# Kernel optimization log

Hardware: AMD Instinct MI355X
Metric: run time of the kernel (lower is better)

## Reference

```python
import jax, jax.numpy as jnp
import numpy as np

HEADS = 8
D_MODEL = 512
HEAD_DIM = D_MODEL // HEADS


def setup_inputs() -> dict:
    key = jax.random.key(0)
    ks = jax.random.split(key, 13)
    B, S, D = 8, 1024, D_MODEL
    scale = 1.0 / np.sqrt(D)
    x = jax.random.normal(ks[0], (B, S, D), dtype=jnp.float32)
    names = ['cq', 'ck', 'cv', 'pq', 'pk', 'pv']
    inp = {'x': x}
    for i, n in enumerate(names):
        inp['W_' + n] = jax.random.normal(ks[1 + 2 * i], (D, D), dtype=jnp.float32) * scale
        inp['b_' + n] = jax.random.normal(ks[2 + 2 * i], (D,), dtype=jnp.float32) * 0.01
    return inp


def reference(x, W_cq, b_cq, W_ck, b_ck, W_cv, b_cv, W_pq, b_pq, W_pk, b_pk, W_pv, b_pv):
    # x: [N, S, D]. Fused common + personal QKV: (x@Wc + bc) + (x@Wp + bp)
    N, S, D = x.shape
    q = x @ (W_cq + W_pq) + (b_cq + b_pq)  # [N, S, D]
    k = x @ (W_ck + W_pk) + (b_ck + b_pk)
    v = x @ (W_cv + W_pv) + (b_cv + b_pv)
    q = q.reshape(N, S, HEADS, HEAD_DIM)
    k = k.reshape(N, S, HEADS, HEAD_DIM)
    v = v.reshape(N, S, HEADS, HEAD_DIM)
    # NOTE: original scales by sqrt(d_model), not sqrt(head_dim)
    energy = jnp.einsum('nqhd,nkhd->nhqk', q, k) / jnp.sqrt(jnp.asarray(D, x.dtype))
    attn = jax.nn.softmax(energy, axis=-1)  # [N, H, Q, K]
    out = jnp.einsum('nhqk,nkhd->nqhd', attn, v).reshape(N, S, D)
    return out
```

## Files before the change

### kernel.cpp

```cpp
#include <hip/hip_runtime.h>

#define B_   8
#define S_   1024
#define D_   512
#define H_   8
#define HD_  64
#define NT_  (B_ * S_)
#define QSCALE_ 0.06376387f
#define C4_    5.7707802f

typedef _Float16 f16;
typedef _Float16 f16x4 __attribute__((ext_vector_type(4)));
typedef _Float16 f16x8 __attribute__((ext_vector_type(8)));
typedef float    f32x4 __attribute__((ext_vector_type(4)));

#define GLOAD_LDS16(g, l) \
    __builtin_amdgcn_global_load_lds( \
        (const __attribute__((address_space(1))) unsigned int*)(g), \
        (__attribute__((address_space(3))) unsigned int*)(l), 16, 0, 0)

#define MFMA16(a, b, c) __builtin_amdgcn_mfma_f32_16x16x32_f16(a, b, c, 0, 0, 0)


__global__ __launch_bounds__(256) void prep_fused(
    const float* __restrict__ x, f16* __restrict__ xh_t,
    const float* __restrict__ Wcq, const float* __restrict__ Wck, const float* __restrict__ Wcv,
    const float* __restrict__ Wpq, const float* __restrict__ Wpk, const float* __restrict__ Wpv,
    f16* __restrict__ Bt_t)
{
    __shared__ float tile[64][68];
    const int tid = threadIdx.x;

    if (blockIdx.x < 1024) {
        const int mtile = blockIdx.x >> 4;
        const int ktile = blockIdx.x & 15;
        f16* dst = xh_t + ((size_t)mtile * 16 + ktile) * 4096;
#pragma unroll
        for (int half = 0; half < 2; ++half) {
            const int q = half * 256 + tid;
            const int r = q >> 2;
            const int c = q & 3;
            const float* src = x + (size_t)(mtile * 128 + r) * D_ + ktile * 32 + c * 8;
            float4 a = *(const float4*)(src);
            float4 b = *(const float4*)(src + 4);
            f16x8 o = { (f16)a.x, (f16)a.y, (f16)a.z, (f16)a.w,
                        (f16)b.x, (f16)b.y, (f16)b.z, (f16)b.w };
            *(f16x8*)(dst + c * 1024 + r * 8) = o;
        }
        return;
    }

    const int wk = blockIdx.x - 1024;
    const int k0 = (wk & 7) * 64;
    const int n0 = (wk >> 3) * 64;
    const int g  = n0 >> 9;
    const int c0 = n0 & 511;
    const float* Wc = (g == 0) ? Wcq : (g == 1) ? Wck : Wcv;
    const float* Wp = (g == 0) ? Wpq : (g == 1) ? Wpk : Wpv;

#pragma unroll
    for (int it = 0; it < 4; ++it) {
        int row = it * 16 + (tid >> 4);
        int c4  = (tid & 15) * 4;
        float4 a = *(const float4*)(Wc + (size_t)(k0 + row) * D_ + c0 + c4);
        float4 b = *(const float4*)(Wp + (size_t)(k0 + row) * D_ + c0 + c4);
        tile[row][c4 + 0] = a.x + b.x;
        tile[row][c4 + 1] = a.y + b.y;
        tile[row][c4 + 2] = a.z + b.z;
        tile[row][c4 + 3] = a.w + b.w;
    }
    __syncthreads();

    const int ntile = n0 >> 7;
    const int rbase = n0 & 64;
#pragma unroll
    for (int it = 0; it < 2; ++it) {
        int nr = it * 32 + (tid >> 3);
        int kc = (tid & 7) * 8;
        f16x8 o;
#pragma unroll
        for (int j = 0; j < 8; ++j) o[j] = (f16)tile[kc + j][nr];
        const int kt = (k0 + kc) >> 5;
        const int c  = (kc >> 3) & 3;
        const int r  = rbase + nr;
        *(f16x8*)(Bt_t + ((size_t)ntile * 16 + kt) * 4096 + c * 1024 + r * 8) = o;
    }
}

__global__ __launch_bounds__(256) void qkv_gemm(
    const f16* __restrict__ xh_t, const f16* __restrict__ Bt_t,
    const float* __restrict__ bcq, const float* __restrict__ bck, const float* __restrict__ bcv,
    const float* __restrict__ bpq, const float* __restrict__ bpk, const float* __restrict__ bpv,
    f16* __restrict__ Qh, f16* __restrict__ Kws, f16* __restrict__ Vws)
{
    __shared__ __align__(16) char smem_raw[36864];

    const int bid   = blockIdx.x;
    const int xcd   = bid & 7;
    const int idx   = bid >> 3;
    const int mtile = xcd * 8 + (idx & 7);
    const int ntile = idx >> 3;
    const int m0 = mtile * 128;
    const int n0 = ntile * 128;

    const int tid  = threadIdx.x;
    const int lane = tid & 63;
    const int wave = tid >> 6;
    const int wr = wave >> 1, wc = wave & 1;
    const int lo4 = lane & 15, hi4 = lane >> 4;

    const f16* gA = xh_t + (size_t)mtile * 16 * 4096;
    const f16* gB = Bt_t + (size_t)ntile * 16 * 4096;

#define STAGE(bufsel, kt) do { \
        f16* _A = (f16*)(smem_raw + (bufsel) * 16384); \
        f16* _B = (f16*)(smem_raw + (bufsel) * 16384 + 8192); \
        GLOAD_LDS16(gA + (kt) * 4096 + tid * 8,         _A + tid * 8);         \
        GLOAD_LDS16(gA + (kt) * 4096 + (tid + 256) * 8, _A + (tid + 256) * 8); \
        GLOAD_LDS16(gB + (kt) * 4096 + tid * 8,         _B + tid * 8);         \
        GLOAD_LDS16(gB + (kt) * 4096 + (tid + 256) * 8, _B + (tid + 256) * 8); \
    } while (0)

    f32x4 acc[4][4];
#pragma unroll
    for (int i = 0; i < 4; ++i)
#pragma unroll
        for (int j = 0; j < 4; ++j) acc[i][j] = (f32x4){0.f, 0.f, 0.f, 0.f};

    STAGE(0, 0);
    asm volatile("s_waitcnt vmcnt(0)" ::: "memory");
    __syncthreads();

    for (int t = 0; t < 16; ++t) {
        const int cur = t & 1;
        if (t < 15) STAGE(cur ^ 1, t + 1);

        const f16* Ab = (const f16*)(smem_raw + cur * 16384);
        const f16* Bb = (const f16*)(smem_raw + cur * 16384 + 8192);
        f16x8 a[4], b[4];
#pragma unroll
        for (int i = 0; i < 4; ++i)
            a[i] = *(const f16x8*)(Ab + hi4 * 1024 + (wr * 64 + i * 16 + lo4) * 8);
#pragma unroll
        for (int j = 0; j < 4; ++j)
            b[j] = *(const f16x8*)(Bb + hi4 * 1024 + (wc * 64 + j * 16 + lo4) * 8);
#pragma unroll
        for (int i = 0; i < 4; ++i)
#pragma unroll
            for (int j = 0; j < 4; ++j)
                acc[i][j] = MFMA16(a[i], b[j], acc[i][j]);

        asm volatile("s_waitcnt vmcnt(0)" ::: "memory");
        __syncthreads();
    }
#undef STAGE

    const int g = n0 >> 9;
    const float* bc = (g == 0) ? bcq : (g == 1) ? bck : bcv;
    const float* bp = (g == 0) ? bpq : (g == 1) ? bpk : bpv;

    const int colb = n0 + wc * 64;
    const int h    = (colb & 511) >> 6;
    const int rowb = m0 + wr * 64;
    const int bb   = rowb >> 10;
    const int s0   = rowb & 1023;

    float bias[4];
#pragma unroll
    for (int j = 0; j < 4; ++j) {
        const int cg = (colb + j * 16 + lo4) & 511;
        bias[j] = bc[cg] + bp[cg];
    }

    f16* Cs = (f16*)smem_raw + wave * 4608;
    const size_t bhbase = (size_t)(bb * H_ + h) * 65536;

    if (g == 2) {
#pragma unroll
        for (int i = 0; i < 4; ++i)
#pragma unroll
            for (int j = 0; j < 4; ++j) {
                f16x4 v = { (f16)(acc[i][j][0] + bias[j]), (f16)(acc[i][j][1] + bias[j]),
                            (f16)(acc[i][j][2] + bias[j]), (f16)(acc[i][j][3] + bias[j]) };
                *(f16x4*)(Cs + (j * 16 + lo4) * 72 + i * 16 + hi4 * 4) = v;
            }
        asm volatile("s_waitcnt lgkmcnt(0)" ::: "memory");
        __builtin_amdgcn_sched_barrier(0);
        const size_t tbase = bhbase + (size_t)(s0 >> 6) * 4096;
#pragma unroll
        for (int it = 0; it < 8; ++it) {
            const int d  = it * 8 + (lane >> 3);
            const int cs = lane & 7;
            f16x8 chunk = *(const f16x8*)(Cs + d * 72 + cs * 8);
            *(f16x8*)(Vws + tbase + d * 64 + ((cs ^ (d & 7)) << 3)) = chunk;
        }
    } else {
        const float scale = (g == 0) ? QSCALE_ : 1.f;
#pragma unroll
        for (int i = 0; i < 4; ++i)
#pragma unroll
            for (int j = 0; j < 4; ++j)
#pragma unroll
                for (int r = 0; r < 4; ++r)
                    Cs[(i * 16 + hi4 * 4 + r) * 72 + j * 16 + lo4] =
                        (f16)((acc[i][j][r] + bias[j]) * scale);
        asm volatile("s_waitcnt lgkmcnt(0)" ::: "memory");
        __builtin_amdgcn_sched_barrier(0);
#pragma unroll
        for (int it = 0; it < 8; ++it) {
            const int rr = it * 8 + (lane >> 3);
            const int ci = lane & 7;
            f16x8 chunk = *(const f16x8*)(Cs + rr * 72 + ci * 8);
            if (g == 0) {
                *(f16x8*)(Qh + bhbase + (size_t)(s0 + rr) * 64 + ci * 8) = chunk;
            } else {
                const size_t tbase = bhbase + (size_t)(s0 >> 6) * 4096;
                *(f16x8*)(Kws + tbase + rr * 64 + ((ci ^ (rr & 7)) << 3)) = chunk;
            }
        }
    }
}

__global__ __launch_bounds__(256) void attn_fwd(
    const f16* __restrict__ Qh, const f16* __restrict__ Kws,
    const f16* __restrict__ Vws, float* __restrict__ out)
{
    __shared__ __align__(16) f16 Ks[2][4096];
    __shared__ __align__(16) f16 Vs[2][4096];
    __shared__ __align__(16) f16 Ps[4][32 * 72];

    const int b0 = blockIdx.x;
    const int bh = (b0 & 7) * 8 + ((b0 >> 3) & 7);
    const int qt = b0 >> 6;

    const int wave = threadIdx.x >> 6;
    const int lane = threadIdx.x & 63;
    const int lo4 = lane & 15, hi4 = lane >> 4;
    const int q0 = qt * 128 + wave * 32;

    const f16* Qp = Qh  + (size_t)bh * 65536;
    const f16* Kp = Kws + (size_t)bh * 65536;
    const f16* Vp = Vws + (size_t)bh * 65536;
    f16* Pw = &Ps[wave][0];

    f16x8 aq[2][2];
#pragma unroll
    for (int qg = 0; qg < 2; ++qg)
#pragma unroll
        for (int hh = 0; hh < 2; ++hh)
            aq[qg][hh] = *(const f16x8*)(Qp + (q0 + qg * 16 + lo4) * 64 + hh * 32 + hi4 * 8);

    f32x4 o[2][4];
    float l[2][4];
#pragma unroll
    for (int qg = 0; qg < 2; ++qg)
#pragma unroll
        for (int dt = 0; dt < 4; ++dt) {
            o[qg][dt] = (f32x4){0.f, 0.f, 0.f, 0.f};
            l[qg][dt] = 0.f;
        }

    const int soff = threadIdx.x * 8;
    GLOAD_LDS16(Kp + soff,        &Ks[0][soff]);
    GLOAD_LDS16(Kp + 2048 + soff, &Ks[0][2048 + soff]);
    GLOAD_LDS16(Vp + soff,        &Vs[0][soff]);
    GLOAD_LDS16(Vp + 2048 + soff, &Vs[0][2048 + soff]);
    asm volatile("s_waitcnt vmcnt(0)" ::: "memory");
    __syncthreads();

    for (int t = 0; t < 16; ++t) {
        const int cur = t & 1;
        if (t < 15) {
            const f16* Kn = Kp + (t + 1) * 4096;
            const f16* Vn = Vp + (t + 1) * 4096;
            GLOAD_LDS16(Kn + soff,        &Ks[cur ^ 1][soff]);
            GLOAD_LDS16(Kn + 2048 + soff, &Ks[cur ^ 1][2048 + soff]);
            GLOAD_LDS16(Vn + soff,        &Vs[cur ^ 1][soff]);
            GLOAD_LDS16(Vn + 2048 + soff, &Vs[cur ^ 1][2048 + soff]);
        }
        const f16* Kc = &Ks[cur][0];
        const f16* Vc = &Vs[cur][0];

#pragma unroll
        for (int f = 0; f < 4; ++f) {
            const int c = f * 16 + lo4;
            f16x8 bk0 = *(const f16x8*)(Kc + c * 64 + ((hi4 ^ (c & 7)) << 3));
            f16x8 bk1 = *(const f16x8*)(Kc + c * 64 + (((4 + hi4) ^ (c & 7)) << 3));
#pragma unroll
            for (int qg = 0; qg < 2; ++qg) {
                f32x4 sc = (f32x4){0.f, 0.f, 0.f, 0.f};
                sc = MFMA16(aq[qg][0], bk0, sc);
                sc = MFMA16(aq[qg][1], bk1, sc);
#pragma unroll
                for (int r = 0; r < 4; ++r) {
                    float p = __builtin_amdgcn_exp2f(sc[r] - C4_);
                    l[qg][r] += p;
                    Pw[(qg * 16 + hi4 * 4 + r) * 72 + f * 16 + lo4] = (f16)p;
                }
            }
        }
        asm volatile("s_waitcnt lgkmcnt(0)" ::: "memory");
        __builtin_amdgcn_sched_barrier(0);

        f16x8 ap[2][2];
#pragma unroll
        for (int qg = 0; qg < 2; ++qg) {
            ap[qg][0] = *(const f16x8*)(Pw + (qg * 16 + lo4) * 72 + hi4 * 8);
            ap[qg][1] = *(const f16x8*)(Pw + (qg * 16 + lo4) * 72 + 32 + hi4 * 8);
        }
#pragma unroll
        for (int dt = 0; dt < 4; ++dt) {
            const int d = dt * 16 + lo4;
            f16x8 bv0 = *(const f16x8*)(Vc + d * 64 + ((hi4 ^ (d & 7)) << 3));
            f16x8 bv1 = *(const f16x8*)(Vc + d * 64 + (((4 + hi4) ^ (d & 7)) << 3));
#pragma unroll
            for (int qg = 0; qg < 2; ++qg) {
                o[qg][dt] = MFMA16(ap[qg][0], bv0, o[qg][dt]);
                o[qg][dt] = MFMA16(ap[qg][1], bv1, o[qg][dt]);
            }
        }

        asm volatile("s_waitcnt vmcnt(0)" ::: "memory");
        __syncthreads();
    }

    const int b = bh >> 3;
    const int h = bh & 7;
#pragma unroll
    for (int qg = 0; qg < 2; ++qg)
#pragma unroll
        for (int r = 0; r < 4; ++r) {
            float lv = l[qg][r];
            lv += __shfl_xor(lv, 1);
            lv += __shfl_xor(lv, 2);
            lv += __shfl_xor(lv, 4);
            lv += __shfl_xor(lv, 8);
            const float inv = 1.f / lv;
            const int s_idx = q0 + qg * 16 + hi4 * 4 + r;
            float* op = out + ((size_t)(b * S_ + s_idx)) * D_ + h * HD_;
#pragma unroll
            for (int dt = 0; dt < 4; ++dt)
                op[dt * 16 + lo4] = o[qg][dt][r] * inv;
        }
}

extern "C" void kernel_launch(void* const* d_in, const int* in_sizes, int n_in,
                              void* d_out, int out_size, void* d_ws, size_t ws_size,
                              hipStream_t stream)
{
    const float* x   = (const float*)d_in[0];
    const float* Wcq = (const float*)d_in[1];
    const float* bcq = (const float*)d_in[2];
    const float* Wck = (const float*)d_in[3];
    const float* bck = (const float*)d_in[4];
    const float* Wcv = (const float*)d_in[5];
    const float* bcv = (const float*)d_in[6];
    const float* Wpq = (const float*)d_in[7];
    const float* bpq = (const float*)d_in[8];
    const float* Wpk = (const float*)d_in[9];
    const float* bpk = (const float*)d_in[10];
    const float* Wpv = (const float*)d_in[11];
    const float* bpv = (const float*)d_in[12];

    f16* ws = (f16*)d_ws;
    f16* xh_t = ws;
    f16* Bt_t = xh_t + (size_t)64 * 16 * 4096;
    f16* Qh   = Bt_t + (size_t)12 * 16 * 4096;
    f16* Kws  = Qh + (size_t)64 * 65536;
    f16* Vws  = Kws + (size_t)64 * 65536;
    float* o = (float*)d_out;

    prep_fused<<<1216, 256, 0, stream>>>(x, xh_t, Wcq, Wck, Wcv, Wpq, Wpk, Wpv, Bt_t);
    qkv_gemm<<<768, 256, 0, stream>>>(xh_t, Bt_t, bcq, bck, bcv, bpq, bpk, bpv,
                                      Qh, Kws, Vws);
    attn_fwd<<<512, 256, 0, stream>>>(Qh, Kws, Vws, o);
}
```

Baseline: 58.02 us.

## Store V transposed and load PV operands directly from global into registers

The QKV GEMM now writes V as a plain per-head transposed [d][s] array instead of swizzled 64x64 tiles. The attention kernel drops the LDS double buffer for V and has each wave read its V operand fragments straight from global memory at the start of each key tile. This frees LDS and cuts the async copy traffic, but every wave now issues its own uncached-in-LDS global loads for V. Those loads are exposed in the loop unless the QK phase hides their latency, and they are redundant across the four waves.

```diff
diff --git a/kernel.cpp b/kernel.cpp
--- a/kernel.cpp
+++ b/kernel.cpp
@@ -91,7 +91,7 @@
     const f16* __restrict__ xh_t, const f16* __restrict__ Bt_t,
     const float* __restrict__ bcq, const float* __restrict__ bck, const float* __restrict__ bcv,
     const float* __restrict__ bpq, const float* __restrict__ bpk, const float* __restrict__ bpv,
-    f16* __restrict__ Qh, f16* __restrict__ Kws, f16* __restrict__ Vws)
+    f16* __restrict__ Qh, f16* __restrict__ Kws, f16* __restrict__ Vt)
 {
     __shared__ __align__(16) char smem_raw[36864];
 
@@ -186,13 +186,12 @@
             }
         asm volatile("s_waitcnt lgkmcnt(0)" ::: "memory");
         __builtin_amdgcn_sched_barrier(0);
-        const size_t tbase = bhbase + (size_t)(s0 >> 6) * 4096;
 #pragma unroll
         for (int it = 0; it < 8; ++it) {
             const int d  = it * 8 + (lane >> 3);
             const int cs = lane & 7;
             f16x8 chunk = *(const f16x8*)(Cs + d * 72 + cs * 8);
-            *(f16x8*)(Vws + tbase + d * 64 + ((cs ^ (d & 7)) << 3)) = chunk;
+            *(f16x8*)(Vt + bhbase + (size_t)d * 1024 + s0 + cs * 8) = chunk;
         }
     } else {
         const float scale = (g == 0) ? QSCALE_ : 1.f;
@@ -223,10 +222,9 @@
 
 __global__ __launch_bounds__(256) void attn_fwd(
     const f16* __restrict__ Qh, const f16* __restrict__ Kws,
-    const f16* __restrict__ Vws, float* __restrict__ out)
+    const f16* __restrict__ Vt, float* __restrict__ out)
 {
     __shared__ __align__(16) f16 Ks[2][4096];
-    __shared__ __align__(16) f16 Vs[2][4096];
     __shared__ __align__(16) f16 Ps[4][32 * 72];
 
     const int b0 = blockIdx.x;
@@ -240,7 +238,7 @@
 
     const f16* Qp = Qh  + (size_t)bh * 65536;
     const f16* Kp = Kws + (size_t)bh * 65536;
-    const f16* Vp = Vws + (size_t)bh * 65536;
+    const f16* Vp = Vt  + (size_t)bh * 65536;
     f16* Pw = &Ps[wave][0];
 
     f16x8 aq[2][2];
@@ -263,8 +261,6 @@
     const int soff = threadIdx.x * 8;
     GLOAD_LDS16(Kp + soff,        &Ks[0][soff]);
     GLOAD_LDS16(Kp + 2048 + soff, &Ks[0][2048 + soff]);
-    GLOAD_LDS16(Vp + soff,        &Vs[0][soff]);
-    GLOAD_LDS16(Vp + 2048 + soff, &Vs[0][2048 + soff]);
     asm volatile("s_waitcnt vmcnt(0)" ::: "memory");
     __syncthreads();
 
@@ -272,14 +268,18 @@
         const int cur = t & 1;
         if (t < 15) {
             const f16* Kn = Kp + (t + 1) * 4096;
-            const f16* Vn = Vp + (t + 1) * 4096;
             GLOAD_LDS16(Kn + soff,        &Ks[cur ^ 1][soff]);
             GLOAD_LDS16(Kn + 2048 + soff, &Ks[cur ^ 1][2048 + soff]);
-            GLOAD_LDS16(Vn + soff,        &Vs[cur ^ 1][soff]);
-            GLOAD_LDS16(Vn + 2048 + soff, &Vs[cur ^ 1][2048 + soff]);
-        }
+        }
+        f16x8 bv[4][2];
+#pragma unroll
+        for (int dt = 0; dt < 4; ++dt)
+#pragma unroll
+            for (int hh = 0; hh < 2; ++hh)
+                bv[dt][hh] = *(const f16x8*)(Vp + (size_t)(dt * 16 + lo4) * 1024
+                                             + t * 64 + hh * 32 + hi4 * 8);
+
         const f16* Kc = &Ks[cur][0];
-        const f16* Vc = &Vs[cur][0];
 
 #pragma unroll
         for (int f = 0; f < 4; ++f) {
@@ -309,16 +309,12 @@
             ap[qg][1] = *(const f16x8*)(Pw + (qg * 16 + lo4) * 72 + 32 + hi4 * 8);
         }
 #pragma unroll
-        for (int dt = 0; dt < 4; ++dt) {
-            const int d = dt * 16 + lo4;
-            f16x8 bv0 = *(const f16x8*)(Vc + d * 64 + ((hi4 ^ (d & 7)) << 3));
-            f16x8 bv1 = *(const f16x8*)(Vc + d * 64 + (((4 + hi4) ^ (d & 7)) << 3));
+        for (int dt = 0; dt < 4; ++dt)
 #pragma unroll
             for (int qg = 0; qg < 2; ++qg) {
-                o[qg][dt] = MFMA16(ap[qg][0], bv0, o[qg][dt]);
-                o[qg][dt] = MFMA16(ap[qg][1], bv1, o[qg][dt]);
+                o[qg][dt] = MFMA16(ap[qg][0], bv[dt][0], o[qg][dt]);
+                o[qg][dt] = MFMA16(ap[qg][1], bv[dt][1], o[qg][dt]);
             }
-        }
 
         asm volatile("s_waitcnt vmcnt(0)" ::: "memory");
         __syncthreads();
@@ -367,11 +363,11 @@
     f16* Bt_t = xh_t + (size_t)64 * 16 * 4096;
     f16* Qh   = Bt_t + (size_t)12 * 16 * 4096;
     f16* Kws  = Qh + (size_t)64 * 65536;
-    f16* Vws  = Kws + (size_t)64 * 65536;
+    f16* Vt   = Kws + (size_t)64 * 65536;
     float* o = (float*)d_out;
 
     prep_fused<<<1216, 256, 0, stream>>>(x, xh_t, Wcq, Wck, Wcv, Wpq, Wpk, Wpv, Bt_t);
     qkv_gemm<<<768, 256, 0, stream>>>(xh_t, Bt_t, bcq, bck, bcv, bpq, bpk, bpv,
-                                      Qh, Kws, Vws);
-    attn_fwd<<<512, 256, 0, stream>>>(Qh, Kws, Vws, o);
+                                      Qh, Kws, Vt);
+    attn_fwd<<<512, 256, 0, stream>>>(Qh, Kws, Vt, o);
 }
```

Measured after the change: 68.25 us. 1.18x slower.
